# Kernel tuning notes

Measured on AMD Instinct MI355X. Metric: run time of the kernel, lower is better.

## Reference

```python
import jax, jax.numpy as jnp
import numpy as np


def _conv(x, w, b=None, stride=1, pad=1, groups=1):
    y = jax.lax.conv_general_dilated(
        x, w, (stride, stride), [(pad, pad), (pad, pad)],
        dimension_numbers=('NCHW', 'OIHW', 'NCHW'), feature_group_count=groups)
    return y if b is None else y + b[None, :, None, None]


def _dwt(x):
    # Haar DWT as grouped stride-2 conv, filters pre-flipped as in the torch code
    ll = np.array([[0.5, 0.5], [0.5, 0.5]])
    lh = np.array([[-0.5, -0.5], [0.5, 0.5]])
    hl = np.array([[-0.5, 0.5], [-0.5, 0.5]])
    hh = np.array([[0.5, -0.5], [-0.5, 0.5]])
    filts = np.stack([f[None, ::-1, ::-1] for f in (ll, lh, hl, hh)], 0)  # [4,1,2,2]
    w = jnp.asarray(np.concatenate([filts] * 3, 0), x.dtype)  # [12,1,2,2], groups=3
    return _conv(x, w, None, stride=2, pad=0, groups=3)


def setup_inputs():
    key = jax.random.key(0)
    ks = iter(jax.random.split(key, 64))
    def w(*shape):
        return jax.random.normal(next(ks), shape, jnp.float32) * 0.05
    B, H, W = 4, 512, 512
    F = 32  # number_f
    d = {'x': jax.random.uniform(next(ks), (B, 3, H, W), jnp.float32)}
    d['enc1_w'] = w(F, 3, 3, 3); d['enc1_b'] = w(F)
    for i in range(2, 6):
        d['enc%d_w' % i] = w(F, F, 3, 3); d['enc%d_b' % i] = w(F)
    d['cdc_w'] = w(F, F, 3, 3)                      # central-difference conv, no bias
    d['ct_w'] = w(64, 9, 3, 3); d['ct_b'] = w(64)   # conv_theta on 9-ch high_freq
    d['t1_w'] = w(64, 64, 1, 1); d['t1_b'] = w(64)
    d['t2_w'] = w(64, 64, 1, 1); d['t2_b'] = w(64)
    d['t3_w'] = w(1, 64, 1, 1); d['t3_b'] = w(1)
    d['lf_w'] = w(64, 3, 3, 3); d['lf_b'] = w(64)   # low_freq conv on haar_A
    d['fc1_w'] = w(512, 64); d['fc1_b'] = w(512)
    d['fc2_w'] = w(512, 512); d['fc2_b'] = w(512)
    d['fc3_w'] = w(512, 512); d['fc3_b'] = w(512)
    d['g_w'] = w(F, 512); d['g_b'] = w(F)           # to_gamma_0
    d['be_w'] = w(F, 512); d['be_b'] = w(F)         # to_beta_0
    d['res_w'] = w(F, F, 3, 3); d['res_b'] = w(F)
    d['d1_w'] = w(F, F, 3, 3); d['d1_b'] = w(F)
    d['d2_w'] = w(1, F, 3, 3); d['d2_b'] = w(1)
    return d


def reference(x, enc1_w, enc1_b, enc2_w, enc2_b, enc3_w, enc3_b, enc4_w, enc4_b,
              enc5_w, enc5_b, cdc_w, ct_w, ct_b, t1_w, t1_b, t2_w, t2_b, t3_w, t3_b,
              lf_w, lf_b, fc1_w, fc1_b, fc2_w, fc2_b, fc3_w, fc3_b,
              g_w, g_b, be_w, be_b, res_w, res_b, d1_w, d1_b, d2_w, d2_b):
    relu = jax.nn.relu
    # encoder
    f = relu(_conv(x, enc1_w, enc1_b))
    f = relu(_conv(f, enc2_w, enc2_b))
    f = relu(_conv(f, enc3_w, enc3_b))
    f = relu(_conv(f, enc4_w, enc4_b))
    f_org4 = relu(_conv(f, enc5_w, enc5_b))  # [B,32,H,W]
    # Haar wavelet split: per input channel blocks of 4 = (A,H,V,D)
    dwt = _dwt(x)                             # [B,12,H/2,W/2]
    haar_A = dwt[:, 0::4]                     # c1,c5,c9
    high_freq = jnp.concatenate([dwt[:, 1::4], dwt[:, 2::4], dwt[:, 3::4]], 1)  # [B,9,...]
    # theta net (Conv2d_cd)
    a = relu(_conv(high_freq, ct_w, ct_b))
    a = a.mean((2, 3), keepdims=True)         # adaptive avg pool to 1x1
    a = relu(_conv(a, t1_w, t1_b, pad=0))
    a = relu(_conv(a, t2_w, t2_b, pad=0))
    theta = jax.nn.sigmoid(_conv(a, t3_w, t3_b, pad=0))   # [B,1,1,1]
    out_normal = _conv(f_org4, cdc_w, None)
    kdiff = cdc_w.sum((2, 3))[:, :, None, None]            # [32,32,1,1]
    out_diff = _conv(f_org4, kdiff, None, pad=0)
    f_deco = relu(out_normal - theta * out_diff)           # [B,32,H,W]
    # attention / FiLM branch
    am = relu(_conv(haar_A, lf_w, lf_b)).mean((2, 3))      # [B,64]
    am = relu(am @ fc1_w.T + fc1_b)
    am = relu(am @ fc2_w.T + fc2_b)
    am = jax.nn.sigmoid(am @ fc3_w.T + fc3_b)              # [B,512]
    gamma = jax.nn.sigmoid(am @ g_w.T + g_b)[:, :, None, None]  # [B,32,1,1]
    beta = jnp.tanh(am @ be_w.T + be_b)[:, :, None, None]
    f = f_deco + gamma * _conv(f_deco, res_w, res_b) + beta
    # decoder
    f = relu(_conv(f, d1_w, d1_b))
    out_map = jnp.tanh(_conv(f, d2_w, d2_b))               # [B,1,H,W]
    enhance_image = x + out_map * (x * x - x)
    return enhance_image, out_map
```

## Files before the change

### kernel.cpp

```cpp
#include <hip/hip_runtime.h>
#include <hip/hip_bf16.h>
#include <cmath>

#define TPB 256

typedef __attribute__((ext_vector_type(8))) short s16x8;
typedef __attribute__((ext_vector_type(4))) float f32x4;
typedef unsigned short ushortT;

constexpr long long PSTR = 8454272;
constexpr int HW = 512 * 512;

static __device__ __forceinline__ short f2bf(float f) {
    union { __hip_bfloat16 h; short s; } u;
    u.h = __float2bfloat16(f);
    return u.s;
}
static __device__ __forceinline__ float bf2f(unsigned short u) {
    union { unsigned int i; float f; } v;
    v.i = ((unsigned int)u) << 16;
    return v.f;
}
static __device__ __forceinline__ unsigned int pack2(float a, float b) {
    return (unsigned int)(unsigned short)f2bf(a) | ((unsigned int)(unsigned short)f2bf(b) << 16);
}

#define GLOAD_LDS16(gp, lp) \
    __builtin_amdgcn_global_load_lds((const __attribute__((address_space(1))) void*)(gp), \
                                     (__attribute__((address_space(3))) void*)(lp), 16, 0, 0)

static __device__ void pack_body(const float* w, const float* bias, const float* theta,
                                 short* dst, int CO, int CI_src, int ci_off, int cog, int l)
{
    const int l15 = l & 15, sl = l >> 4;
    for (int t = 0; t < 9; ++t) {
        for (int mt = 0; mt < 2; ++mt) {
            const int co = cog * 32 + 16 * mt + l15;
            s16x8 p;
            #pragma unroll
            for (int i = 0; i < 8; ++i) {
                const int pci = 8 * sl + i;
                float val = 0.f;
                if (co < CO && pci >= ci_off && pci < ci_off + CI_src) {
                    const int ci = pci - ci_off;
                    val = w[((size_t)co * CI_src + ci) * 9 + t];
                    if (theta && t == 4) {
                        float s = 0.f;
                        for (int tt = 0; tt < 9; ++tt) s += w[((size_t)co * CI_src + ci) * 9 + tt];
                        val -= theta[0] * s;
                    }
                }
                p[i] = f2bf(val);
            }
            *(s16x8*)(dst + ((size_t)(t * 2 + mt) * 64 + l) * 8) = p;
        }
    }
    if (l < 32) {
        const int co = cog * 32 + l;
        ((float*)(dst + 9216))[l] = (bias && co < CO) ? bias[co] : 0.f;
    }
}

__global__ __launch_bounds__(64) void packall_k(
    const float* e1w, const float* e1b, const float* e2w, const float* e2b,
    const float* e3w, const float* e3b, const float* e4w, const float* e4b,
    const float* e5w, const float* e5b, const float* resw, const float* resb,
    const float* d1w, const float* d1b, const float* d2w, const float* d2b,
    const float* ctw, const float* ctb, const float* lfw, const float* lfb,
    short* wpack)
{
    const int s = blockIdx.x;
    const float *w, *b;
    int CO = 32, CI = 32, coff = 0, cog = 0;
    switch (s) {
        case 0: w = e1w; b = e1b; CI = 3; break;
        case 1: w = e2w; b = e2b; break;
        case 2: w = e3w; b = e3b; break;
        case 3: w = e4w; b = e4b; break;
        case 4: w = e5w; b = e5b; break;
        case 5: w = resw; b = resb; break;
        case 6: w = d1w; b = d1b; break;
        case 7: w = d2w; b = d2b; CO = 1; break;
        case 8: case 9: w = ctw; b = ctb; CO = 64; CI = 9; cog = s - 8; break;
        default: w = lfw; b = lfb; CO = 64; CI = 3; coff = 9; cog = s - 10; break;
    }
    pack_body(w, b, nullptr, wpack + (size_t)s * 10240, CO, CI, coff, cog, threadIdx.x);
}

__global__ __launch_bounds__(64) void packcdc_k(
    const float* cdcw, const float* theta, short* wpack)
{
    const int b = blockIdx.x;
    pack_body(cdcw, nullptr, theta + b, wpack + (size_t)(12 + b) * 10240, 32, 32, 0, 0, threadIdx.x);
}

__global__ __launch_bounds__(TPB) void zero_k(unsigned int* A2u, unsigned int* B2u)
{
    const int idx = blockIdx.x * TPB + threadIdx.x;
    if (idx >= 8 * 32832) return;
    const int q = idx / 32832, r = idx % 32832;
    unsigned int* P = (q < 4 ? A2u : B2u) + (size_t)(q & 3) * 4227136;
    const int RSU = 514 * 16;
    int off;
    if (r < 8224)       off = r;
    else if (r < 16448) off = 513 * RSU + (r - 8224);
    else if (r < 24640) { int u = r - 16448; off = (1 + (u >> 4)) * RSU + (u & 15); }
    else                { int u = r - 24640; off = (1 + (u >> 4)) * RSU + 513 * 16 + (u & 15); }
    P[off] = 0u;
}

__global__ __launch_bounds__(TPB) void ctlf_k(
    const float* __restrict__ hf0, const float* __restrict__ haarA0,
    const short* __restrict__ wpack8, float* __restrict__ part)
{
    constexpr int RSX = 66;
    constexpr int ROWB = RSX * 64;
    __shared__ s16x8 lds_t[6 * RSX * 4];
    __shared__ float s_red[4][32];
    char* sb = (char*)lds_t;

    const int z = blockIdx.z, cog = blockIdx.y;
    const int bid = blockIdx.x;
    const int x0 = (bid & 3) * 64, y0 = (bid >> 2) * 4;
    const int tid = threadIdx.x, lane = tid & 63, wv = tid >> 6;
    const int l15 = lane & 15, slot = lane >> 4;

    const short* wslot = wpack8 + (size_t)cog * 10240;
    const float* hfz = hf0 + (size_t)z * 9 * 65536;
    const float* haz = haarA0 + (size_t)z * 3 * 65536;

    s16x8 wf[9][2];
    #pragma unroll
    for (int t = 0; t < 9; ++t)
        #pragma unroll
        for (int mt = 0; mt < 2; ++mt)
            wf[t][mt] = *(const s16x8*)(wslot + ((size_t)(t * 2 + mt) * 64 + lane) * 8);

    #pragma unroll
    for (int j = 0; j < 7; ++j) {
        const int p = j * 256 + tid;
        if (p < 1584) {
            const int row = p / 264;
            const int rem = p - row * 264;
            const int lx = rem >> 2, osl = rem & 3;
            const int o = osl ^ ((lx + (lx >> 2)) & 3);
            s16x8 pk;
            #pragma unroll
            for (int i = 0; i < 8; ++i) pk[i] = 0;
            const int sy = y0 + row - 1, sx = x0 + lx - 1;
            if (o < 2 && sy >= 0 && sy < 256 && sx >= 0 && sx < 256) {
                const size_t base = (size_t)sy * 256 + sx;
                if (o == 0) {
                    #pragma unroll
                    for (int i = 0; i < 8; ++i)
                        pk[i] = f2bf(hfz[(size_t)i * 65536 + base]);
                } else {
                    pk[0] = f2bf(hfz[(size_t)8 * 65536 + base]);
                    pk[1] = f2bf(haz[base]);
                    pk[2] = f2bf(haz[(size_t)65536 + base]);
                    pk[3] = f2bf(haz[(size_t)2 * 65536 + base]);
                }
            }
            *(s16x8*)(sb + p * 16) = pk;
        }
    }
    __syncthreads();

    const int xw = 16 * wv;
    int roff[3];
    #pragma unroll
    for (int dx = 0; dx < 3; ++dx) {
        const int lx = xw + dx + l15;
        const int vs = (lx + (lx >> 2)) & 3;
        roff[dx] = lx * 64 + ((slot ^ vs) << 4);
    }
    const float* bptr = (const float*)(wslot + 9216);

    float ps[2][4];
    #pragma unroll
    for (int mt = 0; mt < 2; ++mt)
        #pragma unroll
        for (int reg = 0; reg < 4; ++reg) ps[mt][reg] = 0.f;

    #pragma unroll
    for (int r2 = 0; r2 < 4; r2 += 2) {
        f32x4 acc[2][2];
        #pragma unroll
        for (int a = 0; a < 2; ++a)
            #pragma unroll
            for (int b = 0; b < 2; ++b)
                #pragma unroll
                for (int e = 0; e < 4; ++e) acc[a][b][e] = 0.f;

        #pragma unroll
        for (int dy = 0; dy < 3; ++dy) {
            const int rb0 = (r2 + dy) * ROWB;
            #pragma unroll
            for (int dx = 0; dx < 3; ++dx) {
                const int tap = dy * 3 + dx;
                const s16x8 b0 = *(const s16x8*)(sb + rb0 + roff[dx]);
                const s16x8 b1 = *(const s16x8*)(sb + rb0 + ROWB + roff[dx]);
                #pragma unroll
                for (int mt = 0; mt < 2; ++mt) {
                    acc[0][mt] = __builtin_amdgcn_mfma_f32_16x16x32_bf16(wf[tap][mt], b0, acc[0][mt], 0, 0, 0);
                    acc[1][mt] = __builtin_amdgcn_mfma_f32_16x16x32_bf16(wf[tap][mt], b1, acc[1][mt], 0, 0, 0);
                }
            }
        }

        #pragma unroll
        for (int rr = 0; rr < 2; ++rr)
            #pragma unroll
            for (int mt = 0; mt < 2; ++mt)
                #pragma unroll
                for (int reg = 0; reg < 4; ++reg)
                    ps[mt][reg] += fmaxf(acc[rr][mt][reg] + bptr[16 * mt + 4 * slot + reg], 0.f);
    }

    #pragma unroll
    for (int mt = 0; mt < 2; ++mt)
        #pragma unroll
        for (int reg = 0; reg < 4; ++reg) {
            #pragma unroll
            for (int o = 1; o < 16; o <<= 1)
                ps[mt][reg] += __shfl_xor(ps[mt][reg], o, 64);
        }
    #pragma unroll
    for (int mt = 0; mt < 2; ++mt)
        #pragma unroll
        for (int reg = 0; reg < 4; ++reg)
            if (l15 == mt * 4 + reg)
                s_red[wv][16 * mt + 4 * slot + reg] = ps[mt][reg];
    __syncthreads();
    if (tid < 32) {
        const float s = s_red[0][tid] + s_red[1][tid] + s_red[2][tid] + s_red[3][tid];
        part[(((size_t)z * 4 + cog) * 256 + bid) * 32 + tid] = s;
    }
}

__global__ __launch_bounds__(TPB) void enc1n_k(
    const float* __restrict__ x0p, const short* __restrict__ wslot,
    ushortT* __restrict__ outP0)
{
    constexpr int RSX = 66;
    constexpr int ROWB = RSX * 64;
    __shared__ s16x8 lds_t[6 * RSX * 4];
    char* sb = (char*)lds_t;

    const int z = blockIdx.z;
    const float* xin = x0p + (size_t)z * 3 * HW;

    const int tid = threadIdx.x, lane = tid & 63, wv = tid >> 6;
    const int bid = blockIdx.x;
    const int swz = (bid & 7) * 128 + (bid >> 3);
    const int x0 = (swz & 7) * 64, y0 = (swz >> 3) * 4;
    const int l15 = lane & 15, slot = lane >> 4;

    s16x8 wf[9][2];
    #pragma unroll
    for (int t = 0; t < 9; ++t)
        #pragma unroll
        for (int mt = 0; mt < 2; ++mt)
            wf[t][mt] = *(const s16x8*)(wslot + ((size_t)(t * 2 + mt) * 64 + lane) * 8);

    #pragma unroll
    for (int j = 0; j < 7; ++j) {
        const int p = j * 256 + tid;
        if (p < 1584) {
            const int row = p / 264;
            const int rem = p - row * 264;
            const int lx = rem >> 2, osl = rem & 3;
            const int o = osl ^ ((lx + (lx >> 2)) & 3);
            s16x8 pk;
            #pragma unroll
            for (int i = 0; i < 8; ++i) pk[i] = 0;
            if (o == 0) {
                const int gy = y0 + row - 1;
                const int gx = x0 + lx - 1;
                if (gy >= 0 && gy < 512 && gx >= 0 && gx < 512) {
                    #pragma unroll
                    for (int c = 0; c < 3; ++c)
                        pk[c] = f2bf(xin[((size_t)c * 512 + gy) * 512 + gx]);
                }
            }
            *(s16x8*)(sb + p * 16) = pk;
        }
    }
    __syncthreads();

    const int xw = 16 * wv;
    int roff[3];
    #pragma unroll
    for (int dx = 0; dx < 3; ++dx) {
        const int lx = xw + dx + l15;
        const int vs = (lx + (lx >> 2)) & 3;
        roff[dx] = lx * 64 + ((slot ^ vs) << 4);
    }
    const float* bptr = (const float*)(wslot + 9216);
    ushortT* outP = outP0 + (size_t)z * PSTR;

    #pragma unroll
    for (int r2 = 0; r2 < 4; r2 += 2) {
        f32x4 acc[2][2];
        #pragma unroll
        for (int a = 0; a < 2; ++a)
            #pragma unroll
            for (int b = 0; b < 2; ++b)
                #pragma unroll
                for (int e = 0; e < 4; ++e) acc[a][b][e] = 0.f;

        #pragma unroll
        for (int dy = 0; dy < 3; ++dy) {
            const int rb0 = (r2 + dy) * ROWB;
            #pragma unroll
            for (int dx = 0; dx < 3; ++dx) {
                const int tap = dy * 3 + dx;
                const s16x8 b0 = *(const s16x8*)(sb + rb0 + roff[dx]);
                const s16x8 b1 = *(const s16x8*)(sb + rb0 + ROWB + roff[dx]);
                #pragma unroll
                for (int mt = 0; mt < 2; ++mt) {
                    acc[0][mt] = __builtin_amdgcn_mfma_f32_16x16x32_bf16(wf[tap][mt], b0, acc[0][mt], 0, 0, 0);
                    acc[1][mt] = __builtin_amdgcn_mfma_f32_16x16x32_bf16(wf[tap][mt], b1, acc[1][mt], 0, 0, 0);
                }
            }
        }

        #pragma unroll
        for (int rr = 0; rr < 2; ++rr) {
            const int gy = y0 + r2 + rr;
            const int gx = x0 + xw + l15;
            #pragma unroll
            for (int mt = 0; mt < 2; ++mt) {
                const size_t off = ((size_t)(gy + 1) * 514 + gx + 1) * 32 + 16 * mt + 4 * slot;
                float v[4];
                #pragma unroll
                for (int reg = 0; reg < 4; ++reg)
                    v[reg] = fmaxf(acc[rr][mt][reg] + bptr[16 * mt + 4 * slot + reg], 0.f);
                *(uint2*)(outP + off) = make_uint2(pack2(v[0], v[1]), pack2(v[2], v[3]));
            }
        }
    }
}

template<int EPI>
__global__ __launch_bounds__(TPB) void dconv64_k(
    const ushortT* __restrict__ inP0, const short* __restrict__ wbase, int wstr,
    ushortT* __restrict__ outP0,
    const float* __restrict__ gamma0, const float* __restrict__ beta0,
    const float* __restrict__ xorig0, float* __restrict__ outE0, float* __restrict__ outM0)
{
    constexpr int MT = (EPI == 3) ? 1 : 2;
    constexpr int RSX = 66;
    constexpr int ROWB = RSX * 64;
    __shared__ s16x8 lds_t[6 * RSX * 4];
    char* sb = (char*)lds_t;

    const int z = blockIdx.z;
    const ushortT* inP = inP0 + (size_t)z * PSTR;
    const short* wslot = wbase + (size_t)z * wstr;

    const int tid = threadIdx.x, lane = tid & 63, wv = tid >> 6;
    const int bid = blockIdx.x;
    const int swz = (bid & 7) * 128 + (bid >> 3);
    const int x0 = (swz & 7) * 64, y0 = (swz >> 3) * 4;
    const int l15 = lane & 15, slot = lane >> 4;

    s16x8 wf[9][MT];
    #pragma unroll
    for (int t = 0; t < 9; ++t)
        #pragma unroll
        for (int mt = 0; mt < MT; ++mt)
            wf[t][mt] = *(const s16x8*)(wslot + ((size_t)(t * 2 + mt) * 64 + lane) * 8);

    #pragma unroll
    for (int j = 0; j < 6; ++j) {
        const int p = j * 256 + tid;
        const int row = p / 264;
        const int rem = p - row * 264;
        const int lx = rem >> 2, osl = rem & 3;
        const int o = osl ^ ((lx + (lx >> 2)) & 3);
        const ushortT* gp = inP + ((size_t)(y0 + row) * 514 + x0 + lx) * 32 + o * 8;
        GLOAD_LDS16(gp, sb + (size_t)(j * 256 + wv * 64) * 16);
    }
    if (tid < 48) {
        const int p = 1536 + tid;
        const int row = p / 264;
        const int rem = p - row * 264;
        const int lx = rem >> 2, osl = rem & 3;
        const int o = osl ^ ((lx + (lx >> 2)) & 3);
        const ushortT* gp = inP + ((size_t)(y0 + row) * 514 + x0 + lx) * 32 + o * 8;
        GLOAD_LDS16(gp, sb + (size_t)1536 * 16);
    }
    __syncthreads();

    const int xw = 16 * wv;
    int roff[3];
    #pragma unroll
    for (int dx = 0; dx < 3; ++dx) {
        const int lx = xw + dx + l15;
        const int vs = (lx + (lx >> 2)) & 3;
        roff[dx] = lx * 64 + ((slot ^ vs) << 4);
    }
    const float* bptr = (const float*)(wslot + 9216);

    #pragma unroll
    for (int r2 = 0; r2 < 4; r2 += 2) {
        f32x4 acc[2][MT];
        #pragma unroll
        for (int a = 0; a < 2; ++a)
            #pragma unroll
            for (int b = 0; b < MT; ++b)
                #pragma unroll
                for (int e = 0; e < 4; ++e) acc[a][b][e] = 0.f;

        #pragma unroll
        for (int dy = 0; dy < 3; ++dy) {
            const int rb0 = (r2 + dy) * ROWB;
            #pragma unroll
            for (int dx = 0; dx < 3; ++dx) {
                const int tap = dy * 3 + dx;
                const s16x8 b0 = *(const s16x8*)(sb + rb0 + roff[dx]);
                const s16x8 b1 = *(const s16x8*)(sb + rb0 + ROWB + roff[dx]);
                #pragma unroll
                for (int mt = 0; mt < MT; ++mt) {
                    acc[0][mt] = __builtin_amdgcn_mfma_f32_16x16x32_bf16(wf[tap][mt], b0, acc[0][mt], 0, 0, 0);
                    acc[1][mt] = __builtin_amdgcn_mfma_f32_16x16x32_bf16(wf[tap][mt], b1, acc[1][mt], 0, 0, 0);
                }
            }
        }

        #pragma unroll
        for (int rr = 0; rr < 2; ++rr) {
            const int gy = y0 + r2 + rr;
            const int gx = x0 + xw + l15;
            if constexpr (EPI == 3) {
                if (slot == 0) {
                    const float* xorig = xorig0 + (size_t)z * 3 * HW;
                    float* outE = outE0 + (size_t)z * 3 * HW;
                    float* outM = outM0 + (size_t)z * HW;
                    const float om = tanhf(acc[rr][0][0] + bptr[0]);
                    outM[(size_t)gy * 512 + gx] = om;
                    #pragma unroll
                    for (int c = 0; c < 3; ++c) {
                        const size_t xi = ((size_t)c * 512 + gy) * 512 + gx;
                        const float xv = xorig[xi];
                        outE[xi] = xv + om * (xv * xv - xv);
                    }
                }
            } else {
                ushortT* outP = outP0 + (size_t)z * PSTR;
                #pragma unroll
                for (int mt = 0; mt < MT; ++mt) {
                    const size_t off = ((size_t)(gy + 1) * 514 + gx + 1) * 32 + 16 * mt + 4 * slot;
                    float v[4];
                    #pragma unroll
                    for (int reg = 0; reg < 4; ++reg)
                        v[reg] = acc[rr][mt][reg] + bptr[16 * mt + 4 * slot + reg];
                    if constexpr (EPI == 0) {
                        #pragma unroll
                        for (int reg = 0; reg < 4; ++reg) v[reg] = fmaxf(v[reg], 0.f);
                    } else if constexpr (EPI == 2) {
                        const int prow = r2 + rr + 1;
                        const int lxr = xw + l15 + 1;
                        const int vsr = (lxr + (lxr >> 2)) & 3;
                        const int oo = (2 * mt + (slot >> 1)) ^ vsr;
                        const uint2 din = *(const uint2*)(sb + (prow * RSX + lxr) * 64 + (oo << 4) + ((slot & 1) << 3));
                        const float* gamma = gamma0 + 32 * z;
                        const float* beta  = beta0 + 32 * z;
                        const int cb = 16 * mt + 4 * slot;
                        v[0] = bf2f((unsigned short)(din.x & 0xffff)) + gamma[cb + 0] * v[0] + beta[cb + 0];
                        v[1] = bf2f((unsigned short)(din.x >> 16))    + gamma[cb + 1] * v[1] + beta[cb + 1];
                        v[2] = bf2f((unsigned short)(din.y & 0xffff)) + gamma[cb + 2] * v[2] + beta[cb + 2];
                        v[3] = bf2f((unsigned short)(din.y >> 16))    + gamma[cb + 3] * v[3] + beta[cb + 3];
                    }
                    *(uint2*)(outP + off) = make_uint2(pack2(v[0], v[1]), pack2(v[2], v[3]));
                }
            }
        }
    }
}

__global__ __launch_bounds__(TPB) void dwt_k(
    const float* __restrict__ x, float* __restrict__ haarA, float* __restrict__ hf)
{
    const int idx = blockIdx.x * TPB + threadIdx.x;
    if (idx >= 4 * 256 * 256) return;
    const int xo = idx & 255;
    const int yo = (idx >> 8) & 255;
    const int b  = idx >> 16;
    #pragma unroll
    for (int c = 0; c < 3; ++c) {
        const float* p = x + (((size_t)b * 3 + c) * 512 + 2 * yo) * 512 + 2 * xo;
        const float a = p[0], bb = p[1], cc = p[512], d = p[513];
        haarA[(((size_t)b * 3 + c) * 256 + yo) * 256 + xo] = 0.5f * (a + bb + cc + d);
        hf[(((size_t)b * 9 + 0 + c) * 256 + yo) * 256 + xo] = 0.5f * (a + bb - cc - d);
        hf[(((size_t)b * 9 + 3 + c) * 256 + yo) * 256 + xo] = 0.5f * (a - bb + cc - d);
        hf[(((size_t)b * 9 + 6 + c) * 256 + yo) * 256 + xo] = 0.5f * (a - bb - cc + d);
    }
}

__global__ __launch_bounds__(TPB) void meanfin_k(
    const float* __restrict__ part, float* __restrict__ amean, float* __restrict__ am0)
{
    const int br = blockIdx.x;
    const int o = threadIdx.x;
    const int z = o >> 6, co = o & 63;
    const int cog = (br ? 2 : 0) + (co >> 5), c = co & 31;
    const float* p = part + (((size_t)z * 4 + cog) * 256) * 32 + c;
    float s = 0.f;
    for (int j = 0; j < 256; ++j) s += p[j * 32];
    (br ? am0 : amean)[z * 64 + co] = s * (1.f / 65536.f);
}

__global__ __launch_bounds__(64) void tchain_k(
    const float* __restrict__ amean,
    const float* __restrict__ t1w, const float* __restrict__ t1b,
    const float* __restrict__ t2w, const float* __restrict__ t2b,
    const float* __restrict__ t3w, const float* __restrict__ t3b,
    float* __restrict__ theta)
{
    const int b = blockIdx.x;
    const float* am = amean + b * 64;
    __shared__ float a0[64], a1[64], a2[64];
    const int co = threadIdx.x;
    a0[co] = am[co];
    __syncthreads();
    float s = t1b[co];
    #pragma unroll 8
    for (int ci = 0; ci < 64; ++ci) s = fmaf(t1w[co * 64 + ci], a0[ci], s);
    a1[co] = fmaxf(s, 0.f);
    __syncthreads();
    s = t2b[co];
    #pragma unroll 8
    for (int ci = 0; ci < 64; ++ci) s = fmaf(t2w[co * 64 + ci], a1[ci], s);
    a2[co] = fmaxf(s, 0.f);
    __syncthreads();
    if (co == 0) {
        float v = t3b[0];
        for (int ci = 0; ci < 64; ++ci) v = fmaf(t3w[ci], a2[ci], v);
        theta[b] = 1.f / (1.f + expf(-v));
    }
}

template<int ACT>
__global__ __launch_bounds__(TPB) void fcw_k(
    const float* __restrict__ in, const float* __restrict__ w,
    const float* __restrict__ bias, float* __restrict__ out, int K, int N)
{
    const int lane = threadIdx.x & 63, wv = threadIdx.x >> 6;
    const int idx = blockIdx.x * 4 + wv;
    if (idx >= 4 * N) return;
    const int b = idx / N, co = idx % N;
    float s = 0.f;
    for (int k = lane * 4; k < K; k += 256) {
        const float4 wv4 = *(const float4*)(w + (size_t)co * K + k);
        const float4 iv  = *(const float4*)(in + (size_t)b * K + k);
        s += wv4.x * iv.x + wv4.y * iv.y + wv4.z * iv.z + wv4.w * iv.w;
    }
    #pragma unroll
    for (int o = 32; o > 0; o >>= 1) s += __shfl_xor(s, o, 64);
    if (lane == 0) {
        s += bias[co];
        if (ACT == 0) s = fmaxf(s, 0.f);
        else if (ACT == 1) s = 1.f / (1.f + expf(-s));
        else s = tanhf(s);
        out[(size_t)b * N + co] = s;
    }
}

extern "C" void kernel_launch(void* const* d_in, const int* in_sizes, int n_in,
                              void* d_out, int out_size, void* d_ws, size_t ws_size,
                              hipStream_t stream)
{
    const float* x      = (const float*)d_in[0];
    const float* cdc_w  = (const float*)d_in[11];
    const float* t1_w   = (const float*)d_in[14];
    const float* t1_b   = (const float*)d_in[15];
    const float* t2_w   = (const float*)d_in[16];
    const float* t2_b   = (const float*)d_in[17];
    const float* t3_w   = (const float*)d_in[18];
    const float* t3_b   = (const float*)d_in[19];
    const float* fc1_w  = (const float*)d_in[22];
    const float* fc1_b  = (const float*)d_in[23];
    const float* fc2_w  = (const float*)d_in[24];
    const float* fc2_b  = (const float*)d_in[25];
    const float* fc3_w  = (const float*)d_in[26];
    const float* fc3_b  = (const float*)d_in[27];
    const float* g_w    = (const float*)d_in[28];
    const float* g_b    = (const float*)d_in[29];
    const float* be_w   = (const float*)d_in[30];
    const float* be_b   = (const float*)d_in[31];

    float* out = (float*)d_out;

    ushortT* A2 = (ushortT*)d_ws;
    ushortT* B2 = A2 + 4 * PSTR;
    float* haarA = (float*)B2;
    float* hf    = haarA + 786432;
    float* part  = (float*)(B2 + 4 * PSTR);
    float* amean = part + 131072;
    float* am0   = amean + 256;
    float* am1   = am0 + 256;
    float* am2   = am1 + 2048;
    float* am3   = am2 + 2048;
    float* theta = am3 + 2048;
    float* gamma = theta + 4;
    float* beta  = gamma + 128;
    short* wpack = (short*)(beta + 128);
    const size_t need_bytes = (size_t)((char*)(wpack + 16 * 10240) - (char*)d_ws);
    if (ws_size < need_bytes) return;

    const dim3 blk(TPB);

    dwt_k<<<dim3((4 * 256 * 256 + TPB - 1) / TPB), blk, 0, stream>>>(x, haarA, hf);
    packall_k<<<dim3(12), dim3(64), 0, stream>>>(
        (const float*)d_in[1], (const float*)d_in[2], (const float*)d_in[3], (const float*)d_in[4],
        (const float*)d_in[5], (const float*)d_in[6], (const float*)d_in[7], (const float*)d_in[8],
        (const float*)d_in[9], (const float*)d_in[10], (const float*)d_in[32], (const float*)d_in[33],
        (const float*)d_in[34], (const float*)d_in[35], (const float*)d_in[36], (const float*)d_in[37],
        (const float*)d_in[12], (const float*)d_in[13], (const float*)d_in[20], (const float*)d_in[21],
        wpack);

    ctlf_k<<<dim3(256, 4, 4), blk, 0, stream>>>(hf, haarA, wpack + 8 * 10240, part);

    zero_k<<<dim3((8 * 32832 + TPB - 1) / TPB), blk, 0, stream>>>((unsigned int*)A2, (unsigned int*)B2);

    meanfin_k<<<dim3(2), blk, 0, stream>>>(part, amean, am0);
    tchain_k<<<dim3(4), dim3(64), 0, stream>>>(amean, t1_w, t1_b, t2_w, t2_b, t3_w, t3_b, theta);
    fcw_k<0><<<dim3(512), blk, 0, stream>>>(am0, fc1_w, fc1_b, am1, 64, 512);
    fcw_k<0><<<dim3(512), blk, 0, stream>>>(am1, fc2_w, fc2_b, am2, 512, 512);
    fcw_k<1><<<dim3(512), blk, 0, stream>>>(am2, fc3_w, fc3_b, am3, 512, 512);
    fcw_k<1><<<dim3(32), blk, 0, stream>>>(am3, g_w, g_b, gamma, 512, 32);
    fcw_k<2><<<dim3(32), blk, 0, stream>>>(am3, be_w, be_b, beta, 512, 32);
    packcdc_k<<<dim3(4), dim3(64), 0, stream>>>(cdc_w, theta, wpack);

    const dim3 gN(1024, 1, 4);
    float* outM = out + (size_t)4 * 3 * HW;

    enc1n_k<<<gN, blk, 0, stream>>>(x, wpack, A2);
    dconv64_k<0><<<gN, blk, 0, stream>>>(A2, wpack + 1 * 10240, 0, B2, nullptr, nullptr, nullptr, nullptr, nullptr);
    dconv64_k<0><<<gN, blk, 0, stream>>>(B2, wpack + 2 * 10240, 0, A2, nullptr, nullptr, nullptr, nullptr, nullptr);
    dconv64_k<0><<<gN, blk, 0, stream>>>(A2, wpack + 3 * 10240, 0, B2, nullptr, nullptr, nullptr, nullptr, nullptr);
    dconv64_k<0><<<gN, blk, 0, stream>>>(B2, wpack + 4 * 10240, 0, A2, nullptr, nullptr, nullptr, nullptr, nullptr);
    dconv64_k<0><<<gN, blk, 0, stream>>>(A2, wpack + 12 * 10240, 10240, B2, nullptr, nullptr, nullptr, nullptr, nullptr);
    dconv64_k<2><<<gN, blk, 0, stream>>>(B2, wpack + 5 * 10240, 0, A2, gamma, beta, nullptr, nullptr, nullptr);
    dconv64_k<0><<<gN, blk, 0, stream>>>(A2, wpack + 6 * 10240, 0, B2, nullptr, nullptr, nullptr, nullptr, nullptr);
    dconv64_k<3><<<gN, blk, 0, stream>>>(B2, wpack + 7 * 10240, 0, nullptr, nullptr, nullptr, x, out, outM);
}
```

Before: 400.5 us.

## Make 3x3 conv blocks persistent over four row tiles with double-buffered LDS staging

Each conv block now handles four consecutive 4-row tiles of a 16-row band instead of one tile. The next tile's input is prefetched into a second LDS buffer while MFMA work runs on the current one. Weight fragments are loaded into registers once per block instead of once per tile, and the grid shrinks from 1024 to 256 blocks per image. The cost is twice the LDS per block, which lowers occupancy. The smaller grid may also leave CUs underused, and there is no explicit wait on the async loads before the barrier.

```diff
diff --git a/kernel.cpp b/kernel.cpp
--- a/kernel.cpp
+++ b/kernel.cpp
@@ -343,7 +343,7 @@
 }
 
 template<int EPI>
-__global__ __launch_bounds__(TPB) void dconv64_k(
+__global__ __launch_bounds__(TPB) void dconv64p_k(
     const ushortT* __restrict__ inP0, const short* __restrict__ wbase, int wstr,
     ushortT* __restrict__ outP0,
     const float* __restrict__ gamma0, const float* __restrict__ beta0,
@@ -352,8 +352,9 @@
     constexpr int MT = (EPI == 3) ? 1 : 2;
     constexpr int RSX = 66;
     constexpr int ROWB = RSX * 64;
-    __shared__ s16x8 lds_t[6 * RSX * 4];
-    char* sb = (char*)lds_t;
+    constexpr int BUFB = 6 * RSX * 64;
+    __shared__ s16x8 lds_t[2 * 6 * RSX * 4];
+    char* sbase = (char*)lds_t;
 
     const int z = blockIdx.z;
     const ushortT* inP = inP0 + (size_t)z * PSTR;
@@ -361,8 +362,9 @@
 
     const int tid = threadIdx.x, lane = tid & 63, wv = tid >> 6;
     const int bid = blockIdx.x;
-    const int swz = (bid & 7) * 128 + (bid >> 3);
-    const int x0 = (swz & 7) * 64, y0 = (swz >> 3) * 4;
+    const int xcd = bid & 7, idx = bid >> 3;
+    const int x0 = (idx & 7) * 64;
+    const int yband = xcd * 4 + (idx >> 3);
     const int l15 = lane & 15, slot = lane >> 4;
 
     s16x8 wf[9][MT];
@@ -371,27 +373,6 @@
         #pragma unroll
         for (int mt = 0; mt < MT; ++mt)
             wf[t][mt] = *(const s16x8*)(wslot + ((size_t)(t * 2 + mt) * 64 + lane) * 8);
-
-    #pragma unroll
-    for (int j = 0; j < 6; ++j) {
-        const int p = j * 256 + tid;
-        const int row = p / 264;
-        const int rem = p - row * 264;
-        const int lx = rem >> 2, osl = rem & 3;
-        const int o = osl ^ ((lx + (lx >> 2)) & 3);
-        const ushortT* gp = inP + ((size_t)(y0 + row) * 514 + x0 + lx) * 32 + o * 8;
-        GLOAD_LDS16(gp, sb + (size_t)(j * 256 + wv * 64) * 16);
-    }
-    if (tid < 48) {
-        const int p = 1536 + tid;
-        const int row = p / 264;
-        const int rem = p - row * 264;
-        const int lx = rem >> 2, osl = rem & 3;
-        const int o = osl ^ ((lx + (lx >> 2)) & 3);
-        const ushortT* gp = inP + ((size_t)(y0 + row) * 514 + x0 + lx) * 32 + o * 8;
-        GLOAD_LDS16(gp, sb + (size_t)1536 * 16);
-    }
-    __syncthreads();
 
     const int xw = 16 * wv;
     int roff[3];
@@ -403,77 +384,111 @@
     }
     const float* bptr = (const float*)(wslot + 9216);
 
-    #pragma unroll
-    for (int r2 = 0; r2 < 4; r2 += 2) {
-        f32x4 acc[2][MT];
-        #pragma unroll
-        for (int a = 0; a < 2; ++a)
-            #pragma unroll
-            for (int b = 0; b < MT; ++b)
-                #pragma unroll
-                for (int e = 0; e < 4; ++e) acc[a][b][e] = 0.f;
-
-        #pragma unroll
-        for (int dy = 0; dy < 3; ++dy) {
-            const int rb0 = (r2 + dy) * ROWB;
-            #pragma unroll
-            for (int dx = 0; dx < 3; ++dx) {
-                const int tap = dy * 3 + dx;
-                const s16x8 b0 = *(const s16x8*)(sb + rb0 + roff[dx]);
-                const s16x8 b1 = *(const s16x8*)(sb + rb0 + ROWB + roff[dx]);
-                #pragma unroll
-                for (int mt = 0; mt < MT; ++mt) {
-                    acc[0][mt] = __builtin_amdgcn_mfma_f32_16x16x32_bf16(wf[tap][mt], b0, acc[0][mt], 0, 0, 0);
-                    acc[1][mt] = __builtin_amdgcn_mfma_f32_16x16x32_bf16(wf[tap][mt], b1, acc[1][mt], 0, 0, 0);
-                }
-            }
-        }
-
-        #pragma unroll
-        for (int rr = 0; rr < 2; ++rr) {
-            const int gy = y0 + r2 + rr;
-            const int gx = x0 + xw + l15;
-            if constexpr (EPI == 3) {
-                if (slot == 0) {
-                    const float* xorig = xorig0 + (size_t)z * 3 * HW;
-                    float* outE = outE0 + (size_t)z * 3 * HW;
-                    float* outM = outM0 + (size_t)z * HW;
-                    const float om = tanhf(acc[rr][0][0] + bptr[0]);
-                    outM[(size_t)gy * 512 + gx] = om;
+    auto stage = [&](int t, int b) {
+        const int y0 = yband * 16 + 4 * t;
+        char* sb = sbase + b * BUFB;
+        #pragma unroll
+        for (int j = 0; j < 6; ++j) {
+            const int p = j * 256 + tid;
+            const int row = p / 264;
+            const int rem = p - row * 264;
+            const int lx = rem >> 2, osl = rem & 3;
+            const int o = osl ^ ((lx + (lx >> 2)) & 3);
+            const ushortT* gp = inP + ((size_t)(y0 + row) * 514 + x0 + lx) * 32 + o * 8;
+            GLOAD_LDS16(gp, sb + (size_t)(j * 256 + wv * 64) * 16);
+        }
+        if (tid < 48) {
+            const int p = 1536 + tid;
+            const int row = p / 264;
+            const int rem = p - row * 264;
+            const int lx = rem >> 2, osl = rem & 3;
+            const int o = osl ^ ((lx + (lx >> 2)) & 3);
+            const ushortT* gp = inP + ((size_t)(y0 + row) * 514 + x0 + lx) * 32 + o * 8;
+            GLOAD_LDS16(gp, sb + (size_t)1536 * 16);
+        }
+    };
+
+    stage(0, 0);
+
+    #pragma unroll 1
+    for (int t = 0; t < 4; ++t) {
+        __syncthreads();
+        if (t < 3) stage(t + 1, (t + 1) & 1);
+        char* sb = sbase + (t & 1) * BUFB;
+        const int y0t = yband * 16 + 4 * t;
+
+        #pragma unroll
+        for (int r2 = 0; r2 < 4; r2 += 2) {
+            f32x4 acc[2][MT];
+            #pragma unroll
+            for (int a = 0; a < 2; ++a)
+                #pragma unroll
+                for (int b = 0; b < MT; ++b)
                     #pragma unroll
-                    for (int c = 0; c < 3; ++c) {
-                        const size_t xi = ((size_t)c * 512 + gy) * 512 + gx;
-                        const float xv = xorig[xi];
-                        outE[xi] = xv + om * (xv * xv - xv);
+                    for (int e = 0; e < 4; ++e) acc[a][b][e] = 0.f;
+
+            #pragma unroll
+            for (int dy = 0; dy < 3; ++dy) {
+                const int rb0 = (r2 + dy) * ROWB;
+                #pragma unroll
+                for (int dx = 0; dx < 3; ++dx) {
+                    const int tap = dy * 3 + dx;
+                    const s16x8 b0 = *(const s16x8*)(sb + rb0 + roff[dx]);
+                    const s16x8 b1 = *(const s16x8*)(sb + rb0 + ROWB + roff[dx]);
+                    #pragma unroll
+                    for (int mt = 0; mt < MT; ++mt) {
+                        acc[0][mt] = __builtin_amdgcn_mfma_f32_16x16x32_bf16(wf[tap][mt], b0, acc[0][mt], 0, 0, 0);
+                        acc[1][mt] = __builtin_amdgcn_mfma_f32_16x16x32_bf16(wf[tap][mt], b1, acc[1][mt], 0, 0, 0);
                     }
                 }
-            } else {
-                ushortT* outP = outP0 + (size_t)z * PSTR;
-                #pragma unroll
-                for (int mt = 0; mt < MT; ++mt) {
-                    const size_t off = ((size_t)(gy + 1) * 514 + gx + 1) * 32 + 16 * mt + 4 * slot;
-                    float v[4];
+            }
+
+            #pragma unroll
+            for (int rr = 0; rr < 2; ++rr) {
+                const int gy = y0t + r2 + rr;
+                const int gx = x0 + xw + l15;
+                if constexpr (EPI == 3) {
+                    if (slot == 0) {
+                        const float* xorig = xorig0 + (size_t)z * 3 * HW;
+                        float* outE = outE0 + (size_t)z * 3 * HW;
+                        float* outM = outM0 + (size_t)z * HW;
+                        const float om = tanhf(acc[rr][0][0] + bptr[0]);
+                        outM[(size_t)gy * 512 + gx] = om;
+                        #pragma unroll
+                        for (int c = 0; c < 3; ++c) {
+                            const size_t xi = ((size_t)c * 512 + gy) * 512 + gx;
+                            const float xv = xorig[xi];
+                            outE[xi] = xv + om * (xv * xv - xv);
+                        }
+                    }
+                } else {
+                    ushortT* outP = outP0 + (size_t)z * PSTR;
                     #pragma unroll
-                    for (int reg = 0; reg < 4; ++reg)
-                        v[reg] = acc[rr][mt][reg] + bptr[16 * mt + 4 * slot + reg];
-                    if constexpr (EPI == 0) {
+                    for (int mt = 0; mt < MT; ++mt) {
+                        const size_t off = ((size_t)(gy + 1) * 514 + gx + 1) * 32 + 16 * mt + 4 * slot;
+                        float v[4];
                         #pragma unroll
-                        for (int reg = 0; reg < 4; ++reg) v[reg] = fmaxf(v[reg], 0.f);
-                    } else if constexpr (EPI == 2) {
-                        const int prow = r2 + rr + 1;
-                        const int lxr = xw + l15 + 1;
-                        const int vsr = (lxr + (lxr >> 2)) & 3;
-                        const int oo = (2 * mt + (slot >> 1)) ^ vsr;
-                        const uint2 din = *(const uint2*)(sb + (prow * RSX + lxr) * 64 + (oo << 4) + ((slot & 1) << 3));
-                        const float* gamma = gamma0 + 32 * z;
-                        const float* beta  = beta0 + 32 * z;
-                        const int cb = 16 * mt + 4 * slot;
-                        v[0] = bf2f((unsigned short)(din.x & 0xffff)) + gamma[cb + 0] * v[0] + beta[cb + 0];
-                        v[1] = bf2f((unsigned short)(din.x >> 16))    + gamma[cb + 1] * v[1] + beta[cb + 1];
-                        v[2] = bf2f((unsigned short)(din.y & 0xffff)) + gamma[cb + 2] * v[2] + beta[cb + 2];
-                        v[3] = bf2f((unsigned short)(din.y >> 16))    + gamma[cb + 3] * v[3] + beta[cb + 3];
+                        for (int reg = 0; reg < 4; ++reg)
+                            v[reg] = acc[rr][mt][reg] + bptr[16 * mt + 4 * slot + reg];
+                        if constexpr (EPI == 0) {
+                            #pragma unroll
+                            for (int reg = 0; reg < 4; ++reg) v[reg] = fmaxf(v[reg], 0.f);
+                        } else if constexpr (EPI == 2) {
+                            const int prow = r2 + rr + 1;
+                            const int lxr = xw + l15 + 1;
+                            const int vsr = (lxr + (lxr >> 2)) & 3;
+                            const int oo = (2 * mt + (slot >> 1)) ^ vsr;
+                            const uint2 din = *(const uint2*)(sb + (prow * RSX + lxr) * 64 + (oo << 4) + ((slot & 1) << 3));
+                            const float* gamma = gamma0 + 32 * z;
+                            const float* beta  = beta0 + 32 * z;
+                            const int cb = 16 * mt + 4 * slot;
+                            v[0] = bf2f((unsigned short)(din.x & 0xffff)) + gamma[cb + 0] * v[0] + beta[cb + 0];
+                            v[1] = bf2f((unsigned short)(din.x >> 16))    + gamma[cb + 1] * v[1] + beta[cb + 1];
+                            v[2] = bf2f((unsigned short)(din.y & 0xffff)) + gamma[cb + 2] * v[2] + beta[cb + 2];
+                            v[3] = bf2f((unsigned short)(din.y >> 16))    + gamma[cb + 3] * v[3] + beta[cb + 3];
+                        }
+                        *(uint2*)(outP + off) = make_uint2(pack2(v[0], v[1]), pack2(v[2], v[3]));
                     }
-                    *(uint2*)(outP + off) = make_uint2(pack2(v[0], v[1]), pack2(v[2], v[3]));
                 }
             }
         }
@@ -634,16 +649,17 @@
     fcw_k<2><<<dim3(32), blk, 0, stream>>>(am3, be_w, be_b, beta, 512, 32);
     packcdc_k<<<dim3(4), dim3(64), 0, stream>>>(cdc_w, theta, wpack);
 
-    const dim3 gN(1024, 1, 4);
+    const dim3 gE(1024, 1, 4);
+    const dim3 gP(256, 1, 4);
     float* outM = out + (size_t)4 * 3 * HW;
 
-    enc1n_k<<<gN, blk, 0, stream>>>(x, wpack, A2);
-    dconv64_k<0><<<gN, blk, 0, stream>>>(A2, wpack + 1 * 10240, 0, B2, nullptr, nullptr, nullptr, nullptr, nullptr);
-    dconv64_k<0><<<gN, blk, 0, stream>>>(B2, wpack + 2 * 10240, 0, A2, nullptr, nullptr, nullptr, nullptr, nullptr);
-    dconv64_k<0><<<gN, blk, 0, stream>>>(A2, wpack + 3 * 10240, 0, B2, nullptr, nullptr, nullptr, nullptr, nullptr);
-    dconv64_k<0><<<gN, blk, 0, stream>>>(B2, wpack + 4 * 10240, 0, A2, nullptr, nullptr, nullptr, nullptr, nullptr);
-    dconv64_k<0><<<gN, blk, 0, stream>>>(A2, wpack + 12 * 10240, 10240, B2, nullptr, nullptr, nullptr, nullptr, nullptr);
-    dconv64_k<2><<<gN, blk, 0, stream>>>(B2, wpack + 5 * 10240, 0, A2, gamma, beta, nullptr, nullptr, nullptr);
-    dconv64_k<0><<<gN, blk, 0, stream>>>(A2, wpack + 6 * 10240, 0, B2, nullptr, nullptr, nullptr, nullptr, nullptr);
-    dconv64_k<3><<<gN, blk, 0, stream>>>(B2, wpack + 7 * 10240, 0, nullptr, nullptr, nullptr, x, out, outM);
-}
+    enc1n_k<<<gE, blk, 0, stream>>>(x, wpack, A2);
+    dconv64p_k<0><<<gP, blk, 0, stream>>>(A2, wpack + 1 * 10240, 0, B2, nullptr, nullptr, nullptr, nullptr, nullptr);
+    dconv64p_k<0><<<gP, blk, 0, stream>>>(B2, wpack + 2 * 10240, 0, A2, nullptr, nullptr, nullptr, nullptr, nullptr);
+    dconv64p_k<0><<<gP, blk, 0, stream>>>(A2, wpack + 3 * 10240, 0, B2, nullptr, nullptr, nullptr, nullptr, nullptr);
+    dconv64p_k<0><<<gP, blk, 0, stream>>>(B2, wpack + 4 * 10240, 0, A2, nullptr, nullptr, nullptr, nullptr, nullptr);
+    dconv64p_k<0><<<gP, blk, 0, stream>>>(A2, wpack + 12 * 10240, 10240, B2, nullptr, nullptr, nullptr, nullptr, nullptr);
+    dconv64p_k<2><<<gP, blk, 0, stream>>>(B2, wpack + 5 * 10240, 0, A2, gamma, beta, nullptr, nullptr, nullptr);
+    dconv64p_k<0><<<gP, blk, 0, stream>>>(A2, wpack + 6 * 10240, 0, B2, nullptr, nullptr, nullptr, nullptr, nullptr);
+    dconv64p_k<3><<<gP, blk, 0, stream>>>(B2, wpack + 7 * 10240, 0, nullptr, nullptr, nullptr, x, out, outM);
+}
```

New measurement: 364.7 us. 8.9% less time.
